# Kernel optimization log

Measured on AMD Instinct MI355X. Metric: run time of the kernel, lower is better.

The kernel has to match this reference:

```python
import jax, jax.numpy as jnp
import numpy as np

B, T, C, FF = 4, 2048, 2048, 8192
EPS_LN = 1e-5
EPS_WKV = 1e-8


def _ln(x, g, b):
    mu = jnp.mean(x, axis=-1, keepdims=True)
    var = jnp.var(x, axis=-1, keepdims=True)
    return (x - mu) * jax.lax.rsqrt(var + EPS_LN) * g + b


def setup_inputs() -> dict:
    key = jax.random.key(0)
    ks = jax.random.split(key, 9)
    w = lambda k, shape: (jax.random.normal(k, shape, jnp.float32) * 0.02)
    return {
        "x": jax.random.normal(ks[0], (B, T, C), jnp.float32),
        "ln1_g": jnp.ones((C,), jnp.float32),
        "ln1_b": jnp.zeros((C,), jnp.float32),
        "time_decay": jax.random.normal(ks[1], (C,), jnp.float32),
        "Wk": w(ks[2], (C, C)),
        "Wv": w(ks[3], (C, C)),
        "Wr": w(ks[4], (C, C)),
        "ln2_g": jnp.ones((C,), jnp.float32),
        "ln2_b": jnp.zeros((C,), jnp.float32),
        "Wck": w(ks[5], (FF, C)),   # key: d_model -> d_ffn
        "Wcv": w(ks[6], (C, FF)),   # value: d_ffn -> d_model
        "Wcr": w(ks[7], (C, C)),    # receptance
    }


def reference(x, ln1_g, ln1_b, time_decay, Wk, Wv, Wr, ln2_g, ln2_b, Wck, Wcv, Wcr):
    # --- TimeMix branch ---
    xln = _ln(x, ln1_g, ln1_b)
    # ZeroPad2d((0,0,1,-1)): shift tokens right by one (zero at t=0, drop last)
    shifted = jnp.pad(xln, ((0, 0), (1, 0), (0, 0)))[:, :-1]  # [B,T,C]
    k = jnp.einsum('btc,dc->btd', shifted, Wk)
    v = jnp.einsum('btc,dc->btd', shifted, Wv)
    r = jnp.einsum('btc,dc->btd', xln, Wr)

    # WKV: exponentially-decayed running weighted average (RWKV linear recurrence)
    decay = jnp.exp(-jnp.exp(time_decay))  # per-channel decay in (0,1)

    def step(carry, kv_t):
        a, b = carry
        k_t, v_t = kv_t
        ek = jnp.exp(k_t)
        a = decay * a + ek * v_t
        b = decay * b + ek
        return (a, b), a / (b + EPS_WKV)

    kT = jnp.swapaxes(k, 0, 1)  # [T,B,C]
    vT = jnp.swapaxes(v, 0, 1)
    init = (jnp.zeros((B, C), x.dtype), jnp.zeros((B, C), x.dtype))
    _, wkvT = jax.lax.scan(step, init, (kT, vT))
    wkv = jnp.swapaxes(wkvT, 0, 1)  # [B,T,C]

    x = x + r * wkv

    # --- ChannelMix branch ---
    x2 = _ln(x, ln2_g, ln2_b)
    ck = jnp.square(jax.nn.relu(jnp.einsum('btc,fc->btf', x2, Wck)))
    dv = jnp.einsum('btf,cf->btc', ck, Wcv)
    cr = jax.nn.sigmoid(jnp.einsum('btc,dc->btd', x2, Wcr))
    x = x + cr * dv

    state = shifted[:, -1]  # [B,C]
    return (x, state)
```

## Files before the change

kernel.cpp:

```cpp
#include <hip/hip_runtime.h>
#include <hip/hip_fp16.h>

typedef unsigned short us;
using short8 = __attribute__((ext_vector_type(8))) short;
using f32x4  = __attribute__((ext_vector_type(4))) float;

#define B_  4
#define T_  2048
#define C_  2048
#define FF_ 8192
#define M_  (B_*T_)
#define NCH 16
#define LCH (T_/NCH)
#define EPS_WKV 1e-8f
#define NK  (C_/64)

__device__ __forceinline__ us f2bf(float f) {
  union { float f; unsigned u; } v; v.f = f;
  return (us)((v.u + 0x7fffu + ((v.u >> 16) & 1u)) >> 16);
}

__device__ __forceinline__ void gload_lds16(const void* g, void* l) {
  __builtin_amdgcn_global_load_lds((__attribute__((address_space(1))) void*)(void*)g,
                                   (__attribute__((address_space(3))) void*)l, 16, 0, 0);
}

__global__ __launch_bounds__(256)
void cvt_bf16(const float* __restrict__ s, us* __restrict__ d) {
  const int i = (blockIdx.x * 256 + threadIdx.x) * 4;
  const float4 v = *(const float4*)(s + i);
  ushort4 o; o.x = f2bf(v.x); o.y = f2bf(v.y); o.z = f2bf(v.z); o.w = f2bf(v.w);
  *(ushort4*)(d + i) = o;
}

__global__ __launch_bounds__(256)
void cvt_bf16_str(const float* __restrict__ s, us* __restrict__ d, int srs) {
  const int row = blockIdx.y;
  const int col = (blockIdx.x * 256 + threadIdx.x) * 4;
  const float4 v = *(const float4*)(s + (size_t)row * srs + col);
  ushort4 o; o.x = f2bf(v.x); o.y = f2bf(v.y); o.z = f2bf(v.z); o.w = f2bf(v.w);
  *(ushort4*)(d + (size_t)row * 2048 + col) = o;
}

template<bool WS>
__global__ __launch_bounds__(256)
void ln_kern(const float* __restrict__ x, const float* __restrict__ g,
             const float* __restrict__ bi, us* __restrict__ y,
             float* __restrict__ state)
{
  const int row = blockIdx.x;
  const int tid = threadIdx.x;
  const float* xr = x + (size_t)row * C_;
  const float4 v0 = ((const float4*)xr)[tid];
  const float4 v1 = ((const float4*)xr)[tid + 256];
  float s  = v0.x + v0.y + v0.z + v0.w + v1.x + v1.y + v1.z + v1.w;
  float sq = v0.x*v0.x + v0.y*v0.y + v0.z*v0.z + v0.w*v0.w
           + v1.x*v1.x + v1.y*v1.y + v1.z*v1.z + v1.w*v1.w;
  #pragma unroll
  for (int o = 32; o > 0; o >>= 1) { s += __shfl_down(s, o, 64); sq += __shfl_down(sq, o, 64); }
  __shared__ float ws_[4], wq_[4];
  if ((tid & 63) == 0) { ws_[tid >> 6] = s; wq_[tid >> 6] = sq; }
  __syncthreads();
  s  = ws_[0] + ws_[1] + ws_[2] + ws_[3];
  sq = wq_[0] + wq_[1] + wq_[2] + wq_[3];
  const float mean = s * (1.f / C_);
  const float rstd = rsqrtf(sq * (1.f / C_) - mean * mean + 1e-5f);
  const float4 g0 = ((const float4*)g)[tid],  g1 = ((const float4*)g)[tid + 256];
  const float4 b0 = ((const float4*)bi)[tid], b1 = ((const float4*)bi)[tid + 256];
  const float o0x = (v0.x - mean) * rstd * g0.x + b0.x;
  const float o0y = (v0.y - mean) * rstd * g0.y + b0.y;
  const float o0z = (v0.z - mean) * rstd * g0.z + b0.z;
  const float o0w = (v0.w - mean) * rstd * g0.w + b0.w;
  const float o1x = (v1.x - mean) * rstd * g1.x + b1.x;
  const float o1y = (v1.y - mean) * rstd * g1.y + b1.y;
  const float o1z = (v1.z - mean) * rstd * g1.z + b1.z;
  const float o1w = (v1.w - mean) * rstd * g1.w + b1.w;
  ushort4 p0; p0.x = f2bf(o0x); p0.y = f2bf(o0y); p0.z = f2bf(o0z); p0.w = f2bf(o0w);
  ushort4 p1; p1.x = f2bf(o1x); p1.y = f2bf(o1y); p1.z = f2bf(o1z); p1.w = f2bf(o1w);
  ((ushort4*)(y + (size_t)row * C_))[tid]       = p0;
  ((ushort4*)(y + (size_t)row * C_))[tid + 256] = p1;
  if (WS && ((row & (T_ - 1)) == (T_ - 2))) {
    float* st = state + (size_t)(row >> 11) * C_;
    const int c0 = tid * 4;
    st[c0 + 0] = o0x; st[c0 + 1] = o0y; st[c0 + 2] = o0z; st[c0 + 3] = o0w;
    st[c0 + 1024 + 0] = o1x; st[c0 + 1024 + 1] = o1y;
    st[c0 + 1024 + 2] = o1z; st[c0 + 1024 + 3] = o1w;
  }
}


#define STAGE_A(D,KB,KO) do { \
  gload_lds16(gA1 + (KO), &lds[(D)*16384 + (KB)*8192 + sdA]); \
  gload_lds16(gA2 + (KO), &lds[(D)*16384 + (KB)*8192 + sdA + 4096]); } while(0)
#define STAGE_B(D,KB,KO) do { \
  gload_lds16(gB1 + (KO), &lds[(D)*16384 + (KB)*8192 + sdB]); \
  gload_lds16(gB2 + (KO), &lds[(D)*16384 + (KB)*8192 + sdB + 4096]); } while(0)

#define LDA_(MF,D,KB) (*(const short8*)&lds[(D)*16384 + (KB)*8192 + (rA + (MF)*16)*32 + cA])
#define LDB_(NF,D,KB) (*(const short8*)&lds[32768 + (D)*16384 + (KB)*8192 + (rB + (NF)*16)*32 + cB])

#define READ_A4(MF0,D,KB) do { _Pragma("unroll") \
  for (int _i = 0; _i < 4; _i++) af[_i] = LDA_((MF0)+_i,(D),(KB)); } while(0)
#define READ_B4(D,KB) do { _Pragma("unroll") \
  for (int _j = 0; _j < 4; _j++) bf[_j] = LDB_(_j,(D),(KB)); } while(0)

#define MFMA16(MF0) do { _Pragma("unroll") \
  for (int _i = 0; _i < 4; _i++) { _Pragma("unroll") \
    for (int _j = 0; _j < 4; _j++) \
      acc[(MF0)+_i][_j] = __builtin_amdgcn_mfma_f32_16x16x32_bf16(af[_i], bf[_j], acc[(MF0)+_i][_j], 0, 0, 0); } } while(0)

#define PH_PRE() do { \
  __builtin_amdgcn_s_barrier(); \
  __builtin_amdgcn_sched_barrier(0); \
  asm volatile("s_waitcnt lgkmcnt(0)" ::: "memory"); \
  __builtin_amdgcn_sched_barrier(0); \
  __builtin_amdgcn_s_setprio(1); } while(0)

#define PH_POST() do { \
  __builtin_amdgcn_s_setprio(0); \
  __builtin_amdgcn_s_barrier(); \
  __builtin_amdgcn_sched_barrier(0); } while(0)

#define PH_POST_VM4() do { \
  __builtin_amdgcn_s_setprio(0); \
  asm volatile("s_waitcnt vmcnt(4)" ::: "memory"); \
  __builtin_amdgcn_s_barrier(); \
  __builtin_amdgcn_sched_barrier(0); } while(0)

#define PH_POST_VM8() do { \
  __builtin_amdgcn_s_setprio(0); \
  asm volatile("s_waitcnt vmcnt(8)" ::: "memory"); \
  __builtin_amdgcn_s_barrier(); \
  __builtin_amdgcn_sched_barrier(0); } while(0)

template<int MODE>
__global__ __launch_bounds__(512, 2)
void gemm_nt(const us* __restrict__ A, const us* __restrict__ Bw,
             void* __restrict__ out0, void* __restrict__ out1, void* __restrict__ out2,
             const __half* __restrict__ crv, float* __restrict__ fout)
{
  __shared__ __align__(16) us lds[65536];
  const int tid  = threadIdx.x;
  const int w    = tid >> 6, l = tid & 63;
  const int quad = l >> 4, l16 = l & 15;
  const int wm = w >> 2, wn = w & 3;
  const size_t m0 = (size_t)blockIdx.y * 256, n0 = (size_t)blockIdx.x * 256;

  const int rA = wm * 128 + l16;
  const int rB = wn * 64  + l16;
  const int cA = (quad ^ ((rA >> 1) & 3)) * 8;
  const int cB = (quad ^ ((rB >> 1) & 3)) * 8;

  const int srow = l >> 2;
  const int scol = ((l & 3) ^ ((l >> 3) & 3)) * 8;
  const us* gA1 = A  + (m0 + (size_t)(w * 16 + srow)) * C_ + scol;
  const us* gA2 = gA1 + (size_t)128 * C_;
  const us* gB1 = Bw + (n0 + (size_t)(w * 16 + srow)) * C_ + scol;
  const us* gB2 = gB1 + (size_t)128 * C_;
  const int sdA = w * 512;
  const int sdB = 32768 + w * 512;

  f32x4 acc[8][4];
  #pragma unroll
  for (int i = 0; i < 8; i++)
    #pragma unroll
    for (int j = 0; j < 4; j++)
      acc[i][j] = (f32x4){0.f, 0.f, 0.f, 0.f};

  short8 af[4], bf[4];

  STAGE_A(0, 0, 0); STAGE_B(0, 0, 0);
  STAGE_A(0, 1, 32); STAGE_B(0, 1, 32);
  asm volatile("s_waitcnt vmcnt(4)" ::: "memory");
  __builtin_amdgcn_s_barrier();
  __builtin_amdgcn_sched_barrier(0);

  int cur = 0;
  #pragma unroll 1
  for (int kt = 0; kt < NK - 1; ++kt) {
    const int nxt = cur ^ 1;
    const int ko  = (kt + 1) * 64;
    READ_A4(0, cur, 0); READ_B4(cur, 0);
    STAGE_A(nxt, 0, ko); STAGE_B(nxt, 0, ko);
    PH_PRE(); MFMA16(0); PH_POST();
    READ_A4(4, cur, 0);
    STAGE_A(nxt, 1, ko + 32); STAGE_B(nxt, 1, ko + 32);
    PH_PRE(); MFMA16(4); PH_POST_VM8();
    READ_A4(0, cur, 1); READ_B4(cur, 1);
    PH_PRE(); MFMA16(0); PH_POST();
    READ_A4(4, cur, 1);
    PH_PRE(); MFMA16(4); PH_POST_VM4();
    cur = nxt;
  }

  READ_A4(0, cur, 0); READ_B4(cur, 0);
  PH_PRE(); MFMA16(0); PH_POST();
  READ_A4(4, cur, 0);
  PH_PRE(); MFMA16(4);
  __builtin_amdgcn_s_setprio(0);
  asm volatile("s_waitcnt vmcnt(0)" ::: "memory");
  __builtin_amdgcn_s_barrier();
  __builtin_amdgcn_sched_barrier(0);
  READ_A4(0, cur, 1); READ_B4(cur, 1);
  PH_PRE(); MFMA16(0); PH_POST();
  READ_A4(4, cur, 1);
  PH_PRE(); MFMA16(4);
  __builtin_amdgcn_s_setprio(0);

  const int nb = (int)(n0 >> 11);
  const size_t ncol0 = n0 - ((size_t)nb << 11);

  #pragma unroll
  for (int mf = 0; mf < 8; mf++) {
    const size_t rbase = m0 + (size_t)(wm * 128 + mf * 16 + quad * 4);
    #pragma unroll
    for (int j = 0; j < 4; j++) {
      const size_t rowoff = (rbase + j) * C_;
      #pragma unroll
      for (int nf = 0; nf < 4; nf++) {
        const size_t nc = (size_t)(wn * 64 + nf * 16 + l16);
        const float v = acc[mf][nf][j];
        if (MODE == 1) {
          const float t = v > 0.f ? v : 0.f;
          ((us*)out0)[rowoff + n0 + nc] = f2bf(t * t);
        } else if (MODE == 2) {
          ((__half*)out0)[rowoff + n0 + nc] = __float2half(1.f / (1.f + expf(-v)));
        } else if (MODE == 3) {
          const size_t idx = rowoff + n0 + nc;
          fout[idx] += (float)crv[idx] * v;
        } else {
          const size_t idx = rowoff + ncol0 + nc;
          if (nb == 0)      ((__half*)out0)[idx] = __float2half(v);
          else if (nb == 1) ((__half*)out1)[idx] = __float2half(v);
          else              ((float*)out2)[idx]  = v;
        }
      }
    }
  }
}

__global__ __launch_bounds__(256)
void wkv_pass1(const __half* __restrict__ Kh, const __half* __restrict__ Vh,
               const float* __restrict__ tdec, float* __restrict__ chA, float* __restrict__ chB)
{
  const int idx = blockIdx.x * 256 + threadIdx.x;
  const int c = idx & (C_ - 1);
  const int chunk = (idx >> 11) & (NCH - 1);
  const int b = idx >> 15;
  const float d = expf(-expf(tdec[c]));
  const size_t base = ((size_t)b * T_) * C_ + c;
  float a = 0.f, bb = 0.f;
  const int t0 = chunk * LCH;
  int t = t0;
  if (chunk == 0) { bb = 1.f; t = 1; }
  const int tend = t0 + LCH;
  #pragma unroll 4
  for (; t < tend; ++t) {
    const size_t off = base + (size_t)(t - 1) * C_;
    const float ek = expf((float)Kh[off]);
    const float vv = (float)Vh[off];
    a  = d * a  + ek * vv;
    bb = d * bb + ek;
  }
  chA[idx] = a; chB[idx] = bb;
}

__global__ __launch_bounds__(256)
void wkv_pass2(const float* __restrict__ tdec, float* __restrict__ chA, float* __restrict__ chB)
{
  const int idx = blockIdx.x * 256 + threadIdx.x;
  const int c = idx & (C_ - 1);
  const int b = idx >> 11;
  const float dL = expf(-expf(tdec[c]) * (float)LCH);
  float a = 0.f, bb = 0.f;
  #pragma unroll
  for (int ch = 0; ch < NCH; ++ch) {
    const int s = (b * NCH + ch) * C_ + c;
    const float la = chA[s], lb = chB[s];
    chA[s] = a; chB[s] = bb;
    a  = dL * a  + la;
    bb = dL * bb + lb;
  }
}

__global__ __launch_bounds__(256)
void wkv_pass3(const __half* __restrict__ Kh, const __half* __restrict__ Vh,
               const float* __restrict__ xin, const float* __restrict__ tdec,
               const float* __restrict__ chA, const float* __restrict__ chB,
               float* __restrict__ outx)
{
  const int idx = blockIdx.x * 256 + threadIdx.x;
  const int c = idx & (C_ - 1);
  const int chunk = (idx >> 11) & (NCH - 1);
  const int b = idx >> 15;
  const float d = expf(-expf(tdec[c]));
  const size_t base = ((size_t)b * T_) * C_ + c;
  float a = chA[idx], bb = chB[idx];
  const int t0 = chunk * LCH;
  int t = t0;
  if (chunk == 0) {
    a = d * a;
    bb = d * bb + 1.f;
    const float wkv = a / (bb + EPS_WKV);
    const float r = outx[base];
    outx[base] = xin[base] + r * wkv;
    t = 1;
  }
  const int tend = t0 + LCH;
  #pragma unroll 4
  for (; t < tend; ++t) {
    const size_t offp = base + (size_t)(t - 1) * C_;
    const size_t off  = base + (size_t)t * C_;
    const float ek = expf((float)Kh[offp]);
    const float vv = (float)Vh[offp];
    a  = d * a  + ek * vv;
    bb = d * bb + ek;
    const float wkv = a / (bb + EPS_WKV);
    const float r = outx[off];
    outx[off] = xin[off] + r * wkv;
  }
}

extern "C" void kernel_launch(void* const* d_in, const int* in_sizes, int n_in,
                              void* d_out, int out_size, void* d_ws, size_t ws_size,
                              hipStream_t stream)
{
  const float* x    = (const float*)d_in[0];
  const float* ln1g = (const float*)d_in[1];
  const float* ln1b = (const float*)d_in[2];
  const float* tdec = (const float*)d_in[3];
  const float* Wk   = (const float*)d_in[4];
  const float* Wv   = (const float*)d_in[5];
  const float* Wr   = (const float*)d_in[6];
  const float* ln2g = (const float*)d_in[7];
  const float* ln2b = (const float*)d_in[8];
  const float* Wck  = (const float*)d_in[9];
  const float* Wcv  = (const float*)d_in[10];
  const float* Wcr  = (const float*)d_in[11];

  char* ws = (char*)d_ws;
  us*     xln  = (us*)(ws);
  __half* Kb   = (__half*)(ws + (32ull  << 20));
  __half* Vb   = (__half*)(ws + (64ull  << 20));
  float*  chA  = (float*)(ws + (96ull << 20));
  float*  chB  = (float*)(ws + (96ull << 20) + 524288ull);
  us*     wkvr = (us*)(ws + (97ull  << 20));
  us*     wcrb = (us*)(ws + (121ull << 20));
  us*     wckc = (us*)(ws + (129ull << 20));
  us*     wcvc = (us*)(ws + (137ull << 20));
  us*     x2   = (us*)Kb;
  __half* crb  = (__half*)Vb;
  us*     ckc  = (us*)xln;

  float* outx = (float*)d_out;
  float* outs = outx + (size_t)M_ * C_;

  const dim3 blk(256);
  const dim3 blkG(512);
  const dim3 gC(C_ / 256, M_ / 256);
  const dim3 gKVR(3 * C_ / 256, M_ / 256);

  cvt_bf16<<<4096, blk, 0, stream>>>(Wk,  wkvr);
  cvt_bf16<<<4096, blk, 0, stream>>>(Wv,  wkvr + (size_t)C_ * C_);
  cvt_bf16<<<4096, blk, 0, stream>>>(Wr,  wkvr + 2 * (size_t)C_ * C_);
  cvt_bf16<<<4096, blk, 0, stream>>>(Wcr, wcrb);

  ln_kern<true><<<M_, blk, 0, stream>>>(x, ln1g, ln1b, xln, outs);

  gemm_nt<5><<<gKVR, blkG, 0, stream>>>(xln, wkvr, (void*)Kb, (void*)Vb, (void*)outx, nullptr, nullptr);

  wkv_pass1<<<(B_ * NCH * C_) / 256, blk, 0, stream>>>(Kb, Vb, tdec, chA, chB);
  wkv_pass2<<<(B_ * C_) / 256,       blk, 0, stream>>>(tdec, chA, chB);
  wkv_pass3<<<(B_ * NCH * C_) / 256, blk, 0, stream>>>(Kb, Vb, x, tdec, chA, chB, outx);

  ln_kern<false><<<M_, blk, 0, stream>>>(outx, ln2g, ln2b, x2, nullptr);

  gemm_nt<2><<<gC, blkG, 0, stream>>>(x2, wcrb, (void*)crb, nullptr, nullptr, nullptr, nullptr);

  for (int f0 = 0; f0 < FF_; f0 += 2048) {
    cvt_bf16<<<4096, blk, 0, stream>>>(Wck + (size_t)f0 * C_, wckc);
    gemm_nt<1><<<gC, blkG, 0, stream>>>(x2, wckc, (void*)ckc, nullptr, nullptr, nullptr, nullptr);
    cvt_bf16_str<<<dim3(2, 2048), blk, 0, stream>>>(Wcv + f0, wcvc, FF_);
    gemm_nt<3><<<gC, blkG, 0, stream>>>(ckc, wcvc, nullptr, nullptr, nullptr, crb, outx);
  }
}
```

Measured before the change: 1.314 ms.

## Switch GEMM inner loop to 32x32x16 bf16 MFMA with merged phases

After: 1.343 ms. +2.2%, slower.

```diff
diff --git a/kernel.cpp b/kernel.cpp
--- a/kernel.cpp
+++ b/kernel.cpp
@@ -3,7 +3,7 @@
 
 typedef unsigned short us;
 using short8 = __attribute__((ext_vector_type(8))) short;
-using f32x4  = __attribute__((ext_vector_type(4))) float;
+using f32x16 = __attribute__((ext_vector_type(16))) float;
 
 #define B_  4
 #define T_  2048
@@ -96,18 +96,20 @@
   gload_lds16(gB1 + (KO), &lds[(D)*16384 + (KB)*8192 + sdB]); \
   gload_lds16(gB2 + (KO), &lds[(D)*16384 + (KB)*8192 + sdB + 4096]); } while(0)
 
-#define LDA_(MF,D,KB) (*(const short8*)&lds[(D)*16384 + (KB)*8192 + (rA + (MF)*16)*32 + cA])
-#define LDB_(NF,D,KB) (*(const short8*)&lds[32768 + (D)*16384 + (KB)*8192 + (rB + (NF)*16)*32 + cB])
-
-#define READ_A4(MF0,D,KB) do { _Pragma("unroll") \
-  for (int _i = 0; _i < 4; _i++) af[_i] = LDA_((MF0)+_i,(D),(KB)); } while(0)
-#define READ_B4(D,KB) do { _Pragma("unroll") \
-  for (int _j = 0; _j < 4; _j++) bf[_j] = LDB_(_j,(D),(KB)); } while(0)
-
-#define MFMA16(MF0) do { _Pragma("unroll") \
-  for (int _i = 0; _i < 4; _i++) { _Pragma("unroll") \
-    for (int _j = 0; _j < 4; _j++) \
-      acc[(MF0)+_i][_j] = __builtin_amdgcn_mfma_f32_16x16x32_bf16(af[_i], bf[_j], acc[(MF0)+_i][_j], 0, 0, 0); } } while(0)
+#define LDA32(MF,D,KB,CC) (*(const short8*)&lds[(D)*16384 + (KB)*8192 + (rA32 + (MF)*32)*32 + (CC)])
+#define LDB32(NF,D,KB,CC) (*(const short8*)&lds[32768 + (D)*16384 + (KB)*8192 + (rB32 + (NF)*32)*32 + (CC)])
+
+#define READ_PH(D,KB) do { \
+  _Pragma("unroll") for (int _m = 0; _m < 4; _m++) af[_m][0] = LDA32(_m,(D),(KB),cS0); \
+  _Pragma("unroll") for (int _m = 0; _m < 4; _m++) af[_m][1] = LDA32(_m,(D),(KB),cS1); \
+  bf[0][0] = LDB32(0,(D),(KB),cS0); bf[1][0] = LDB32(1,(D),(KB),cS0); \
+  bf[0][1] = LDB32(0,(D),(KB),cS1); bf[1][1] = LDB32(1,(D),(KB),cS1); } while(0)
+
+#define MFMA_PH() do { _Pragma("unroll") \
+  for (int _s = 0; _s < 2; _s++) { _Pragma("unroll") \
+    for (int _m = 0; _m < 4; _m++) { _Pragma("unroll") \
+      for (int _n = 0; _n < 2; _n++) \
+        acc[_m][_n] = __builtin_amdgcn_mfma_f32_32x32x16_bf16(af[_m][_s], bf[_n][_s], acc[_m][_n], 0, 0, 0); } } } while(0)
 
 #define PH_PRE() do { \
   __builtin_amdgcn_s_barrier(); \
@@ -116,23 +118,12 @@
   __builtin_amdgcn_sched_barrier(0); \
   __builtin_amdgcn_s_setprio(1); } while(0)
 
-#define PH_POST() do { \
-  __builtin_amdgcn_s_setprio(0); \
-  __builtin_amdgcn_s_barrier(); \
-  __builtin_amdgcn_sched_barrier(0); } while(0)
-
 #define PH_POST_VM4() do { \
   __builtin_amdgcn_s_setprio(0); \
   asm volatile("s_waitcnt vmcnt(4)" ::: "memory"); \
   __builtin_amdgcn_s_barrier(); \
   __builtin_amdgcn_sched_barrier(0); } while(0)
 
-#define PH_POST_VM8() do { \
-  __builtin_amdgcn_s_setprio(0); \
-  asm volatile("s_waitcnt vmcnt(8)" ::: "memory"); \
-  __builtin_amdgcn_s_barrier(); \
-  __builtin_amdgcn_sched_barrier(0); } while(0)
-
 template<int MODE>
 __global__ __launch_bounds__(512, 2)
 void gemm_nt(const us* __restrict__ A, const us* __restrict__ Bw,
@@ -142,14 +133,15 @@
   __shared__ __align__(16) us lds[65536];
   const int tid  = threadIdx.x;
   const int w    = tid >> 6, l = tid & 63;
-  const int quad = l >> 4, l16 = l & 15;
+  const int l31  = l & 31, hi = l >> 5;
   const int wm = w >> 2, wn = w & 3;
   const size_t m0 = (size_t)blockIdx.y * 256, n0 = (size_t)blockIdx.x * 256;
 
-  const int rA = wm * 128 + l16;
-  const int rB = wn * 64  + l16;
-  const int cA = (quad ^ ((rA >> 1) & 3)) * 8;
-  const int cB = (quad ^ ((rB >> 1) & 3)) * 8;
+  const int rA32 = wm * 128 + l31;
+  const int rB32 = wn * 64  + l31;
+  const int sw   = (l31 >> 1) & 3;
+  const int cS0  = ((hi ^ sw)) * 8;
+  const int cS1  = (((2 + hi) ^ sw)) * 8;
 
   const int srow = l >> 2;
   const int scol = ((l & 3) ^ ((l >> 3) & 3)) * 8;
@@ -160,14 +152,14 @@
   const int sdA = w * 512;
   const int sdB = 32768 + w * 512;
 
-  f32x4 acc[8][4];
+  f32x16 acc[4][2];
   #pragma unroll
-  for (int i = 0; i < 8; i++)
+  for (int i = 0; i < 4; i++)
     #pragma unroll
-    for (int j = 0; j < 4; j++)
-      acc[i][j] = (f32x4){0.f, 0.f, 0.f, 0.f};
-
-  short8 af[4], bf[4];
+    for (int j = 0; j < 2; j++)
+      acc[i][j] = (f32x16)(0.f);
+
+  short8 af[4][2], bf[2][2];
 
   STAGE_A(0, 0, 0); STAGE_B(0, 0, 0);
   STAGE_A(0, 1, 32); STAGE_B(0, 1, 32);
@@ -180,59 +172,55 @@
   for (int kt = 0; kt < NK - 1; ++kt) {
     const int nxt = cur ^ 1;
     const int ko  = (kt + 1) * 64;
-    READ_A4(0, cur, 0); READ_B4(cur, 0);
+    READ_PH(cur, 0);
     STAGE_A(nxt, 0, ko); STAGE_B(nxt, 0, ko);
-    PH_PRE(); MFMA16(0); PH_POST();
-    READ_A4(4, cur, 0);
+    PH_PRE(); MFMA_PH(); PH_POST_VM4();
+    READ_PH(cur, 1);
     STAGE_A(nxt, 1, ko + 32); STAGE_B(nxt, 1, ko + 32);
-    PH_PRE(); MFMA16(4); PH_POST_VM8();
-    READ_A4(0, cur, 1); READ_B4(cur, 1);
-    PH_PRE(); MFMA16(0); PH_POST();
-    READ_A4(4, cur, 1);
-    PH_PRE(); MFMA16(4); PH_POST_VM4();
+    PH_PRE(); MFMA_PH(); PH_POST_VM4();
     cur = nxt;
   }
 
-  READ_A4(0, cur, 0); READ_B4(cur, 0);
-  PH_PRE(); MFMA16(0); PH_POST();
-  READ_A4(4, cur, 0);
-  PH_PRE(); MFMA16(4);
+  READ_PH(cur, 0);
+  PH_PRE(); MFMA_PH();
   __builtin_amdgcn_s_setprio(0);
   asm volatile("s_waitcnt vmcnt(0)" ::: "memory");
   __builtin_amdgcn_s_barrier();
   __builtin_amdgcn_sched_barrier(0);
-  READ_A4(0, cur, 1); READ_B4(cur, 1);
-  PH_PRE(); MFMA16(0); PH_POST();
-  READ_A4(4, cur, 1);
-  PH_PRE(); MFMA16(4);
+  READ_PH(cur, 1);
+  PH_PRE(); MFMA_PH();
   __builtin_amdgcn_s_setprio(0);
 
   const int nb = (int)(n0 >> 11);
   const size_t ncol0 = n0 - ((size_t)nb << 11);
 
   #pragma unroll
-  for (int mf = 0; mf < 8; mf++) {
-    const size_t rbase = m0 + (size_t)(wm * 128 + mf * 16 + quad * 4);
+  for (int mf = 0; mf < 4; mf++) {
     #pragma unroll
-    for (int j = 0; j < 4; j++) {
-      const size_t rowoff = (rbase + j) * C_;
+    for (int nf = 0; nf < 2; nf++) {
+      const size_t nc = (size_t)(wn * 64 + nf * 32 + l31);
       #pragma unroll
-      for (int nf = 0; nf < 4; nf++) {
-        const size_t nc = (size_t)(wn * 64 + nf * 16 + l16);
-        const float v = acc[mf][nf][j];
-        if (MODE == 1) {
-          const float t = v > 0.f ? v : 0.f;
-          ((us*)out0)[rowoff + n0 + nc] = f2bf(t * t);
-        } else if (MODE == 2) {
-          ((__half*)out0)[rowoff + n0 + nc] = __float2half(1.f / (1.f + expf(-v)));
-        } else if (MODE == 3) {
-          const size_t idx = rowoff + n0 + nc;
-          fout[idx] += (float)crv[idx] * v;
-        } else {
-          const size_t idx = rowoff + ncol0 + nc;
-          if (nb == 0)      ((__half*)out0)[idx] = __float2half(v);
-          else if (nb == 1) ((__half*)out1)[idx] = __float2half(v);
-          else              ((float*)out2)[idx]  = v;
+      for (int rg = 0; rg < 4; rg++) {
+        #pragma unroll
+        for (int rj = 0; rj < 4; rj++) {
+          const int r = rg * 4 + rj;
+          const size_t row = m0 + (size_t)(wm * 128 + mf * 32 + rg * 8 + rj + 4 * hi);
+          const size_t rowoff = row * C_;
+          const float v = acc[mf][nf][r];
+          if (MODE == 1) {
+            const float t = v > 0.f ? v : 0.f;
+            ((us*)out0)[rowoff + n0 + nc] = f2bf(t * t);
+          } else if (MODE == 2) {
+            ((__half*)out0)[rowoff + n0 + nc] = __float2half(1.f / (1.f + expf(-v)));
+          } else if (MODE == 3) {
+            const size_t idx = rowoff + n0 + nc;
+            fout[idx] += (float)crv[idx] * v;
+          } else {
+            const size_t idx = rowoff + ncol0 + nc;
+            if (nb == 0)      ((__half*)out0)[idx] = __float2half(v);
+            else if (nb == 1) ((__half*)out1)[idx] = __float2half(v);
+            else              ((float*)out2)[idx]  = v;
+          }
         }
       }
     }
```

## Merge GEMM MFMA phases per k-half and double WKV scan chunks

Applied to the files above, without the earlier changes.

Measured after the change: 1.218 ms. 7.3% less time.

```diff
diff --git a/kernel.cpp b/kernel.cpp
--- a/kernel.cpp
+++ b/kernel.cpp
@@ -10,7 +10,8 @@
 #define C_  2048
 #define FF_ 8192
 #define M_  (B_*T_)
-#define NCH 16
+#define NCHB 5
+#define NCH (1<<NCHB)
 #define LCH (T_/NCH)
 #define EPS_WKV 1e-8f
 #define NK  (C_/64)
@@ -99,15 +100,14 @@
 #define LDA_(MF,D,KB) (*(const short8*)&lds[(D)*16384 + (KB)*8192 + (rA + (MF)*16)*32 + cA])
 #define LDB_(NF,D,KB) (*(const short8*)&lds[32768 + (D)*16384 + (KB)*8192 + (rB + (NF)*16)*32 + cB])
 
-#define READ_A4(MF0,D,KB) do { _Pragma("unroll") \
-  for (int _i = 0; _i < 4; _i++) af[_i] = LDA_((MF0)+_i,(D),(KB)); } while(0)
-#define READ_B4(D,KB) do { _Pragma("unroll") \
-  for (int _j = 0; _j < 4; _j++) bf[_j] = LDB_(_j,(D),(KB)); } while(0)
-
-#define MFMA16(MF0) do { _Pragma("unroll") \
-  for (int _i = 0; _i < 4; _i++) { _Pragma("unroll") \
+#define READ_PH2(D,KB) do { \
+  _Pragma("unroll") for (int _i = 0; _i < 8; _i++) af[_i] = LDA_(_i,(D),(KB)); \
+  _Pragma("unroll") for (int _j = 0; _j < 4; _j++) bf[_j] = LDB_(_j,(D),(KB)); } while(0)
+
+#define MFMA32() do { _Pragma("unroll") \
+  for (int _i = 0; _i < 8; _i++) { _Pragma("unroll") \
     for (int _j = 0; _j < 4; _j++) \
-      acc[(MF0)+_i][_j] = __builtin_amdgcn_mfma_f32_16x16x32_bf16(af[_i], bf[_j], acc[(MF0)+_i][_j], 0, 0, 0); } } while(0)
+      acc[_i][_j] = __builtin_amdgcn_mfma_f32_16x16x32_bf16(af[_i], bf[_j], acc[_i][_j], 0, 0, 0); } } while(0)
 
 #define PH_PRE() do { \
   __builtin_amdgcn_s_barrier(); \
@@ -116,20 +116,9 @@
   __builtin_amdgcn_sched_barrier(0); \
   __builtin_amdgcn_s_setprio(1); } while(0)
 
-#define PH_POST() do { \
-  __builtin_amdgcn_s_setprio(0); \
-  __builtin_amdgcn_s_barrier(); \
-  __builtin_amdgcn_sched_barrier(0); } while(0)
-
 #define PH_POST_VM4() do { \
   __builtin_amdgcn_s_setprio(0); \
   asm volatile("s_waitcnt vmcnt(4)" ::: "memory"); \
-  __builtin_amdgcn_s_barrier(); \
-  __builtin_amdgcn_sched_barrier(0); } while(0)
-
-#define PH_POST_VM8() do { \
-  __builtin_amdgcn_s_setprio(0); \
-  asm volatile("s_waitcnt vmcnt(8)" ::: "memory"); \
   __builtin_amdgcn_s_barrier(); \
   __builtin_amdgcn_sched_barrier(0); } while(0)
 
@@ -154,9 +143,9 @@
   const int srow = l >> 2;
   const int scol = ((l & 3) ^ ((l >> 3) & 3)) * 8;
   const us* gA1 = A  + (m0 + (size_t)(w * 16 + srow)) * C_ + scol;
-  const us* gA2 = gA1 + (size_t)128 * C_;
+  const us* gA2 = gA1 + (size_t)64 * C_ * 2;
   const us* gB1 = Bw + (n0 + (size_t)(w * 16 + srow)) * C_ + scol;
-  const us* gB2 = gB1 + (size_t)128 * C_;
+  const us* gB2 = gB1 + (size_t)64 * C_ * 2;
   const int sdA = w * 512;
   const int sdB = 32768 + w * 512;
 
@@ -167,7 +156,7 @@
     for (int j = 0; j < 4; j++)
       acc[i][j] = (f32x4){0.f, 0.f, 0.f, 0.f};
 
-  short8 af[4], bf[4];
+  short8 af[8], bf[4];
 
   STAGE_A(0, 0, 0); STAGE_B(0, 0, 0);
   STAGE_A(0, 1, 32); STAGE_B(0, 1, 32);
@@ -180,31 +169,23 @@
   for (int kt = 0; kt < NK - 1; ++kt) {
     const int nxt = cur ^ 1;
     const int ko  = (kt + 1) * 64;
-    READ_A4(0, cur, 0); READ_B4(cur, 0);
+    READ_PH2(cur, 0);
     STAGE_A(nxt, 0, ko); STAGE_B(nxt, 0, ko);
-    PH_PRE(); MFMA16(0); PH_POST();
-    READ_A4(4, cur, 0);
+    PH_PRE(); MFMA32(); PH_POST_VM4();
+    READ_PH2(cur, 1);
     STAGE_A(nxt, 1, ko + 32); STAGE_B(nxt, 1, ko + 32);
-    PH_PRE(); MFMA16(4); PH_POST_VM8();
-    READ_A4(0, cur, 1); READ_B4(cur, 1);
-    PH_PRE(); MFMA16(0); PH_POST();
-    READ_A4(4, cur, 1);
-    PH_PRE(); MFMA16(4); PH_POST_VM4();
+    PH_PRE(); MFMA32(); PH_POST_VM4();
     cur = nxt;
   }
 
-  READ_A4(0, cur, 0); READ_B4(cur, 0);
-  PH_PRE(); MFMA16(0); PH_POST();
-  READ_A4(4, cur, 0);
-  PH_PRE(); MFMA16(4);
+  READ_PH2(cur, 0);
+  PH_PRE(); MFMA32();
   __builtin_amdgcn_s_setprio(0);
   asm volatile("s_waitcnt vmcnt(0)" ::: "memory");
   __builtin_amdgcn_s_barrier();
   __builtin_amdgcn_sched_barrier(0);
-  READ_A4(0, cur, 1); READ_B4(cur, 1);
-  PH_PRE(); MFMA16(0); PH_POST();
-  READ_A4(4, cur, 1);
-  PH_PRE(); MFMA16(4);
+  READ_PH2(cur, 1);
+  PH_PRE(); MFMA32();
   __builtin_amdgcn_s_setprio(0);
 
   const int nb = (int)(n0 >> 11);
@@ -246,7 +227,7 @@
   const int idx = blockIdx.x * 256 + threadIdx.x;
   const int c = idx & (C_ - 1);
   const int chunk = (idx >> 11) & (NCH - 1);
-  const int b = idx >> 15;
+  const int b = idx >> (11 + NCHB);
   const float d = expf(-expf(tdec[c]));
   const size_t base = ((size_t)b * T_) * C_ + c;
   float a = 0.f, bb = 0.f;
@@ -292,7 +273,7 @@
   const int idx = blockIdx.x * 256 + threadIdx.x;
   const int c = idx & (C_ - 1);
   const int chunk = (idx >> 11) & (NCH - 1);
-  const int b = idx >> 15;
+  const int b = idx >> (11 + NCHB);
   const float d = expf(-expf(tdec[c]));
   const size_t base = ((size_t)b * T_) * C_ + c;
   float a = chA[idx], bb = chB[idx];
@@ -342,9 +323,9 @@
   us*     xln  = (us*)(ws);
   __half* Kb   = (__half*)(ws + (32ull  << 20));
   __half* Vb   = (__half*)(ws + (64ull  << 20));
-  float*  chA  = (float*)(ws + (96ull << 20));
-  float*  chB  = (float*)(ws + (96ull << 20) + 524288ull);
   us*     wkvr = (us*)(ws + (97ull  << 20));
+  float*  chA  = (float*)(ws + (97ull << 20));
+  float*  chB  = (float*)(ws + (98ull << 20));
   us*     wcrb = (us*)(ws + (121ull << 20));
   us*     wckc = (us*)(ws + (129ull << 20));
   us*     wcvc = (us*)(ws + (137ull << 20));
```
